# Kernel tuning notes

Hardware: AMD Instinct MI355X
Metric: run time of the kernel (lower is better)

The kernel has to match this reference:

```python
import jax, jax.numpy as jnp
import numpy as np

B, L = 4, 2048
D_MODEL, D_STATE, D_CONV, N_BLOCKS = 128, 16, 8, 6
EXPAND = 2
D_INNER = EXPAND * D_MODEL          # 256
DT_RANK = (D_MODEL + 15) // 16      # 8
CONV_K = 7                          # pre_conv kernel


def setup_inputs() -> dict:
    key = jax.random.key(0)
    ks = jax.random.split(key, 10)
    f = lambda k, s: jax.random.normal(k, s, jnp.float32)
    sc = 0.02
    A_init = jnp.broadcast_to(
        jnp.log(jnp.arange(1, D_STATE + 1, dtype=jnp.float32)),
        (N_BLOCKS, D_INNER, D_STATE)) + 0.0
    return {
        "x": f(ks[0], (B, L, 1)),
        "pre_conv_w": f(ks[1], (D_MODEL, 1, CONV_K)) * sc,
        "pre_conv_b": jnp.zeros((D_MODEL,), jnp.float32),
        "ln_w": jnp.ones((N_BLOCKS, D_MODEL), jnp.float32),
        "ln_b": jnp.zeros((N_BLOCKS, D_MODEL), jnp.float32),
        "W_in": f(ks[2], (N_BLOCKS, 2 * D_INNER, D_MODEL)) * sc,
        "conv_w": f(ks[3], (N_BLOCKS, D_INNER, 1, D_CONV)) * sc,  # depthwise OIH
        "conv_b": jnp.zeros((N_BLOCKS, D_INNER), jnp.float32),
        "W_x": f(ks[4], (N_BLOCKS, DT_RANK + 2 * D_STATE, D_INNER)) * sc,
        "W_dt": f(ks[5], (N_BLOCKS, D_INNER, DT_RANK)) * sc,
        "b_dt": jnp.full((N_BLOCKS, D_INNER), -4.6, jnp.float32),  # softplus ~ 0.01
        "A_log": A_init,
        "D_skip": jnp.ones((N_BLOCKS, D_INNER), jnp.float32),
        "W_out": f(ks[6], (N_BLOCKS, D_MODEL, D_INNER)) * sc,
        "out_w": f(ks[7], (1, D_MODEL)) * sc,
        "out_b": jnp.zeros((1,), jnp.float32),
    }


def _layernorm(x, w, b, eps=1e-5):
    m = jnp.mean(x, axis=-1, keepdims=True)
    v = jnp.mean(jnp.square(x - m), axis=-1, keepdims=True)
    return (x - m) * jax.lax.rsqrt(v + eps) * w + b


def _mamba(x, W_in, cw, cb, W_x, W_dt, b_dt, A_log, D_skip, W_out):
    # x: (B, L, D_MODEL)
    xz = jnp.einsum('bld,ed->ble', x, W_in)            # (B,L,2E)
    xi, z = jnp.split(xz, 2, axis=-1)
    # depthwise causal conv over time
    xc = jax.lax.conv_general_dilated(
        xi.transpose(0, 2, 1), cw, window_strides=(1,),
        padding=[(D_CONV - 1, 0)],
        dimension_numbers=('NCH', 'OIH', 'NCH'),
        feature_group_count=D_INNER) + cb[None, :, None]
    xc = jax.nn.silu(xc).transpose(0, 2, 1)            # (B,L,E)
    dbl = jnp.einsum('ble,re->blr', xc, W_x)
    dt = dbl[..., :DT_RANK]
    Bm = dbl[..., DT_RANK:DT_RANK + D_STATE]           # (B,L,N)
    Cm = dbl[..., DT_RANK + D_STATE:]                  # (B,L,N)
    delta = jax.nn.softplus(jnp.einsum('blr,er->ble', dt, W_dt) + b_dt)
    A = -jnp.exp(A_log)                                # (E,N)

    def step(h, inp):
        d, b, c, u = inp                               # (B,E),(B,N),(B,N),(B,E)
        h = h * jnp.exp(d[..., None] * A) + (d * u)[..., None] * b[:, None, :]
        return h, jnp.einsum('ben,bn->be', h, c)

    h0 = jnp.zeros((x.shape[0], D_INNER, D_STATE), x.dtype)
    xs = (delta.transpose(1, 0, 2), Bm.transpose(1, 0, 2),
          Cm.transpose(1, 0, 2), xc.transpose(1, 0, 2))
    _, ys = jax.lax.scan(step, h0, xs)                 # ys: (L,B,E)
    y = ys.transpose(1, 0, 2) + D_skip * xc
    y = y * jax.nn.silu(z)
    return jnp.einsum('ble,de->bld', y, W_out)


def reference(x, pre_conv_w, pre_conv_b, ln_w, ln_b, W_in, conv_w, conv_b,
              W_x, W_dt, b_dt, A_log, D_skip, W_out, out_w, out_b):
    # pre_conv (1 -> d_model), SAME padding, then exact GELU
    h = jax.lax.conv_general_dilated(
        x.transpose(0, 2, 1), pre_conv_w, window_strides=(1,),
        padding=[(CONV_K // 2, CONV_K // 2)],
        dimension_numbers=('NCH', 'OIH', 'NCH')) + pre_conv_b[None, :, None]
    h = jax.nn.gelu(h, approximate=False).transpose(0, 2, 1)  # (B,L,D)

    def block(carry, p):
        lw, lb, Wi, cw, cb, Wx, Wdt, bdt, Alog, Dsk, Wo = p
        y = _mamba(_layernorm(carry, lw, lb), Wi, cw, cb, Wx, Wdt, bdt, Alog, Dsk, Wo)
        return carry + y, None                         # dropout is identity (eval)

    h, _ = jax.lax.scan(block, h, (ln_w, ln_b, W_in, conv_w, conv_b,
                                   W_x, W_dt, b_dt, A_log, D_skip, W_out))
    return (jnp.einsum('bld,od->blo', h, out_w) + out_b)[..., 0]  # (B,L)
```

## Files before the change

kernel.cpp:

```cpp
#include <hip/hip_runtime.h>
#include <hip/hip_bf16.h>
#include <math.h>

#define BB 4
#define LL 2048
#define DM 128
#define DI 256
#define DS 16
#define DTR 8
#define NB 6
#define KPRE 7
#define KC 8
#define NC 64
#define CT 32
#define BL (BB*LL)
#define SU 4

typedef __attribute__((ext_vector_type(8))) short short8v;
typedef __attribute__((ext_vector_type(4))) float f32x4;

__global__ void k_preconv_gelu(const float* __restrict__ x,
                               const float* __restrict__ w,
                               const float* __restrict__ bias,
                               float* __restrict__ h,
                               const float* __restrict__ Wi,
                               const float* __restrict__ Wo,
                               __hip_bfloat16* __restrict__ wi,
                               __hip_bfloat16* __restrict__ wo) {
    int tid = blockIdx.x * blockDim.x + threadIdx.x;
    int d = tid & (DM - 1);
    int l = (tid >> 7) & (LL - 1);
    int b = tid >> 18;
    float acc = bias[d];
#pragma unroll
    for (int k = 0; k < KPRE; ++k) {
        int pos = l + k - 3;
        float xv = (pos >= 0 && pos < LL) ? x[b * LL + pos] : 0.f;
        acc = fmaf(xv, w[d * KPRE + k], acc);
    }
    h[tid] = 0.5f * acc * (1.f + erff(acc * 0.70710678118654752f));
    if (tid < NB * 2 * DI * DM) wi[tid] = __float2bfloat16(Wi[tid]);
    if (tid < NB * DM * DI)     wo[tid] = __float2bfloat16(Wo[tid]);
}

__global__ __launch_bounds__(256) void k_ln_gemm1(const float* __restrict__ h,
                                                  const float* __restrict__ lw,
                                                  const float* __restrict__ lb,
                                                  const __hip_bfloat16* __restrict__ W,
                                                  float* __restrict__ xz) {
    __shared__ __hip_bfloat16 As[128 * 128];
    int wave = threadIdx.x >> 6;
    int lane = threadIdx.x & 63;
    int mBase = blockIdx.x * 128;
    int nBase = blockIdx.y * 128;
    for (int it = 0; it < 32; ++it) {
        int row = wave * 32 + it;
        int t = mBase + row;
        float v0 = h[t * DM + lane];
        float v1 = h[t * DM + lane + 64];
        float s = v0 + v1;
#pragma unroll
        for (int off = 32; off; off >>= 1) s += __shfl_xor(s, off);
        float mean = s * (1.f / 128.f);
        float d0 = v0 - mean, d1 = v1 - mean;
        float q = d0 * d0 + d1 * d1;
#pragma unroll
        for (int off = 32; off; off >>= 1) q += __shfl_xor(q, off);
        float rstd = rsqrtf(q * (1.f / 128.f) + 1e-5f);
        int sw = (row & 7) << 3;
        As[row * 128 + (lane ^ sw)]        = __float2bfloat16(d0 * rstd * lw[lane] + lb[lane]);
        As[row * 128 + ((lane + 64) ^ sw)] = __float2bfloat16(d1 * rstd * lw[lane + 64] + lb[lane + 64]);
    }
    __syncthreads();
    int wm = wave & 1, wn = wave >> 1;
    int r  = lane & 15;
    int kh = lane >> 4;
    f32x4 acc[4][4] = {};
    for (int k0 = 0; k0 < DM; k0 += 32) {
        short8v af[4], bf[4];
#pragma unroll
        for (int i = 0; i < 4; ++i) {
            int row = wm * 64 + i * 16 + r;
            int cbk = (k0 >> 3) + kh;
            af[i] = *(const short8v*)&As[row * 128 + ((cbk ^ (row & 7)) << 3)];
            bf[i] = *(const short8v*)&W[(size_t)(nBase + wn * 64 + i * 16 + r) * DM + k0 + kh * 8];
        }
#pragma unroll
        for (int i = 0; i < 4; ++i)
#pragma unroll
            for (int j = 0; j < 4; ++j)
                acc[i][j] = __builtin_amdgcn_mfma_f32_16x16x32_bf16(af[i], bf[j], acc[i][j], 0, 0, 0);
    }
#pragma unroll
    for (int i = 0; i < 4; ++i)
#pragma unroll
        for (int j = 0; j < 4; ++j)
#pragma unroll
            for (int rg = 0; rg < 4; ++rg) {
                size_t off = (size_t)(mBase + wm * 64 + i * 16 + kh * 4 + rg) * (2 * DI)
                           + nBase + wn * 64 + j * 16 + r;
                xz[off] = acc[i][j][rg];
            }
}

__global__ __launch_bounds__(256) void k_gemm2_mfma(const __hip_bfloat16* __restrict__ A,
                                                    const __hip_bfloat16* __restrict__ W,
                                                    float* __restrict__ C) {
    int wave = threadIdx.x >> 6;
    int lane = threadIdx.x & 63;
    int wm = wave & 1, wn = wave >> 1;
    int mBase = blockIdx.x * 32 + wm * 16;
    int nBase = wn * 64;
    int r  = lane & 15;
    int kh = lane >> 4;
    f32x4 acc[4] = {};
    for (int k0 = 0; k0 < DI; k0 += 32) {
        short8v af = *(const short8v*)&A[(size_t)(mBase + r) * DI + k0 + kh * 8];
        short8v bf[4];
#pragma unroll
        for (int j = 0; j < 4; ++j)
            bf[j] = *(const short8v*)&W[(size_t)(nBase + j * 16 + r) * DI + k0 + kh * 8];
#pragma unroll
        for (int j = 0; j < 4; ++j)
            acc[j] = __builtin_amdgcn_mfma_f32_16x16x32_bf16(af, bf[j], acc[j], 0, 0, 0);
    }
#pragma unroll
    for (int j = 0; j < 4; ++j)
#pragma unroll
        for (int rg = 0; rg < 4; ++rg) {
            size_t off = (size_t)(mBase + kh * 4 + rg) * DM + nBase + j * 16 + r;
            C[off] += acc[j][rg];
        }
}

__global__ __launch_bounds__(256) void k_conv_wx(const float* __restrict__ xz,
                                                 const float* __restrict__ cw,
                                                 const float* __restrict__ cbs,
                                                 const float* __restrict__ Wx,
                                                 const float* __restrict__ Wdt,
                                                 const float* __restrict__ bdt,
                                                 float* __restrict__ xc,
                                                 float* __restrict__ BC,
                                                 float* __restrict__ delta) {
    int lane = threadIdx.x & 63;
    int t = blockIdx.x * 4 + (threadIdx.x >> 6);
    int tl = t & (LL - 1);
    int b = t >> 11;
    float xv[4];
#pragma unroll
    for (int j = 0; j < 4; ++j) {
        int e = lane + 64 * j;
        float4 cw0 = *(const float4*)&cw[e * KC];
        float4 cw1 = *(const float4*)&cw[e * KC + 4];
        float wts[8] = {cw0.x, cw0.y, cw0.z, cw0.w, cw1.x, cw1.y, cw1.z, cw1.w};
        float acc = cbs[e];
#pragma unroll
        for (int k = 0; k < KC; ++k) {
            int pos = tl + k - (KC - 1);
            float v = (pos >= 0) ? xz[((size_t)(b * LL + pos) << 9) + e] : 0.f;
            acc = fmaf(v, wts[k], acc);
        }
        xv[j] = acc / (1.f + __expf(-acc));
        xc[((size_t)t << 8) + e] = xv[j];
    }
    float dt[8];
    float bcv = 0.f;
#pragma unroll
    for (int o = 0; o < 40; ++o) {
        const float* w = &Wx[o * DI];
        float s = xv[0] * w[lane];
        s = fmaf(xv[1], w[lane + 64], s);
        s = fmaf(xv[2], w[lane + 128], s);
        s = fmaf(xv[3], w[lane + 192], s);
#pragma unroll
        for (int off = 32; off; off >>= 1) s += __shfl_xor(s, off);
        if (o < 8) dt[o] = s;
        else if (lane == o - 8) bcv = s;
    }
    if (lane < 32) BC[((size_t)t << 5) + lane] = bcv;
#pragma unroll
    for (int j = 0; j < 4; ++j) {
        int e = lane + 64 * j;
        float s = bdt[e];
#pragma unroll
        for (int r = 0; r < 8; ++r) s = fmaf(dt[r], Wdt[e * 8 + r], s);
        delta[((size_t)t << 8) + e] = fmaxf(s, 0.f) + log1pf(__expf(-fabsf(s)));
    }
}

__global__ __launch_bounds__(256) void k_scan1(const float* __restrict__ delta,
                                               const float* __restrict__ xc,
                                               const float* __restrict__ BC,
                                               const float* __restrict__ A_log,
                                               float* __restrict__ P,
                                               float* __restrict__ hend) {
    int blk = blockIdx.x;
    int eg = blk & 3;
    int c = (blk >> 2) & (NC - 1);
    int b = blk >> 8;
    int tid = threadIdx.x;
    int e = eg * 64 + (tid >> 2);
    int ng = tid & 3;
    float4 al = *(const float4*)&A_log[e * DS + 4 * ng];
    float Aen[4] = {-__expf(al.x), -__expf(al.y), -__expf(al.z), -__expf(al.w)};
    float h[4] = {}, Pl[4] = {1.f, 1.f, 1.f, 1.f};
    int base = b * LL + c * CT;
    const float* dp = delta + (size_t)base * DI + e;
    const float* up = xc + (size_t)base * DI + e;
    const float* bp = BC + (size_t)base * 32 + 4 * ng;
    for (int l0 = 0; l0 < CT; l0 += SU) {
        float d[SU], u[SU];
        float4 bm[SU];
#pragma unroll
        for (int j = 0; j < SU; ++j) {
            d[j]  = dp[(l0 + j) * DI];
            u[j]  = up[(l0 + j) * DI];
            bm[j] = *(const float4*)&bp[(l0 + j) * 32];
        }
#pragma unroll
        for (int j = 0; j < SU; ++j) {
            float du = d[j] * u[j];
            float a0 = __expf(d[j] * Aen[0]);
            float a1 = __expf(d[j] * Aen[1]);
            float a2 = __expf(d[j] * Aen[2]);
            float a3 = __expf(d[j] * Aen[3]);
            h[0] = fmaf(h[0], a0, du * bm[j].x);
            h[1] = fmaf(h[1], a1, du * bm[j].y);
            h[2] = fmaf(h[2], a2, du * bm[j].z);
            h[3] = fmaf(h[3], a3, du * bm[j].w);
            Pl[0] *= a0; Pl[1] *= a1; Pl[2] *= a2; Pl[3] *= a3;
        }
    }
    size_t oidx = (((size_t)(b * NC + c)) * DI + e) * DS + 4 * ng;
    *(float4*)&P[oidx]    = make_float4(Pl[0], Pl[1], Pl[2], Pl[3]);
    *(float4*)&hend[oidx] = make_float4(h[0], h[1], h[2], h[3]);
}

__global__ void k_scan_carry(const float* __restrict__ P,
                             const float* __restrict__ hend,
                             float* __restrict__ hin) {
    int tid = blockIdx.x * blockDim.x + threadIdx.x;
    int n = tid & 15;
    int e = (tid >> 4) & 255;
    int b = tid >> 12;
    float carry = 0.f;
    for (int c = 0; c < NC; ++c) {
        size_t idx = (((size_t)(b * NC + c)) * DI + e) * DS + n;
        hin[idx] = carry;
        carry = fmaf(P[idx], carry, hend[idx]);
    }
}

__global__ __launch_bounds__(256) void k_scan3(const float* __restrict__ delta,
                                               const float* __restrict__ xc,
                                               const float* __restrict__ BC,
                                               const float* __restrict__ A_log,
                                               const float* __restrict__ hin,
                                               const float* __restrict__ xz,
                                               const float* __restrict__ Dsk,
                                               __hip_bfloat16* __restrict__ y) {
    int blk = blockIdx.x;
    int eg = blk & 3;
    int c = (blk >> 2) & (NC - 1);
    int b = blk >> 8;
    int tid = threadIdx.x;
    int e = eg * 64 + (tid >> 2);
    int ng = tid & 3;
    float4 al = *(const float4*)&A_log[e * DS + 4 * ng];
    float Aen[4] = {-__expf(al.x), -__expf(al.y), -__expf(al.z), -__expf(al.w)};
    float dsk = Dsk[e];
    size_t hidx = (((size_t)(b * NC + c)) * DI + e) * DS + 4 * ng;
    float4 h4 = *(const float4*)&hin[hidx];
    float h[4] = {h4.x, h4.y, h4.z, h4.w};
    int base = b * LL + c * CT;
    const float* dp = delta + (size_t)base * DI + e;
    const float* up = xc + (size_t)base * DI + e;
    const float* bp = BC + (size_t)base * 32 + 4 * ng;
    const float* zp = xz + ((size_t)base << 9) + DI + e;
    __hip_bfloat16* yp = y + (size_t)base * DI + e;
    for (int l0 = 0; l0 < CT; l0 += SU) {
        float d[SU], u[SU], zv[SU];
        float4 bm[SU], cm[SU];
#pragma unroll
        for (int j = 0; j < SU; ++j) {
            d[j]  = dp[(l0 + j) * DI];
            u[j]  = up[(l0 + j) * DI];
            bm[j] = *(const float4*)&bp[(l0 + j) * 32];
            cm[j] = *(const float4*)&bp[(l0 + j) * 32 + 16];
            zv[j] = zp[(size_t)(l0 + j) << 9];
        }
#pragma unroll
        for (int j = 0; j < SU; ++j) {
            float du = d[j] * u[j];
            float a0 = __expf(d[j] * Aen[0]);
            float a1 = __expf(d[j] * Aen[1]);
            float a2 = __expf(d[j] * Aen[2]);
            float a3 = __expf(d[j] * Aen[3]);
            h[0] = fmaf(h[0], a0, du * bm[j].x);
            h[1] = fmaf(h[1], a1, du * bm[j].y);
            h[2] = fmaf(h[2], a2, du * bm[j].z);
            h[3] = fmaf(h[3], a3, du * bm[j].w);
            float yc = h[0] * cm[j].x;
            yc = fmaf(h[1], cm[j].y, yc);
            yc = fmaf(h[2], cm[j].z, yc);
            yc = fmaf(h[3], cm[j].w, yc);
            yc += __shfl_xor(yc, 1);
            yc += __shfl_xor(yc, 2);
            if (ng == 0) {
                float z = zv[j];
                float val = (yc + dsk * u[j]) * (z / (1.f + __expf(-z)));
                yp[(l0 + j) * DI] = __float2bfloat16(val);
            }
        }
    }
}

__global__ void k_out(const float* __restrict__ h,
                      const float* __restrict__ ow,
                      const float* __restrict__ ob,
                      float* __restrict__ out) {
    int t = blockIdx.x * 4 + (threadIdx.x >> 6);
    int lane = threadIdx.x & 63;
    float s = h[t * DM + lane] * ow[lane] + h[t * DM + lane + 64] * ow[lane + 64];
#pragma unroll
    for (int off = 32; off; off >>= 1) s += __shfl_xor(s, off);
    if (lane == 0) out[t] = s + ob[0];
}

extern "C" void kernel_launch(void* const* d_in, const int* in_sizes, int n_in,
                              void* d_out, int out_size, void* d_ws, size_t ws_size,
                              hipStream_t stream) {
    (void)in_sizes; (void)n_in; (void)out_size; (void)ws_size;
    const float* x      = (const float*)d_in[0];
    const float* pcw    = (const float*)d_in[1];
    const float* pcb    = (const float*)d_in[2];
    const float* ln_w   = (const float*)d_in[3];
    const float* ln_b   = (const float*)d_in[4];
    const float* W_in   = (const float*)d_in[5];
    const float* conv_w = (const float*)d_in[6];
    const float* conv_b = (const float*)d_in[7];
    const float* W_x    = (const float*)d_in[8];
    const float* W_dt   = (const float*)d_in[9];
    const float* b_dt   = (const float*)d_in[10];
    const float* A_log  = (const float*)d_in[11];
    const float* D_skip = (const float*)d_in[12];
    const float* W_out  = (const float*)d_in[13];
    const float* out_w  = (const float*)d_in[14];
    const float* out_b  = (const float*)d_in[15];

    float* ws    = (float*)d_ws;
    float* h     = ws;
    float* xz    = h     + (size_t)BL * DM;
    float* xc    = xz    + (size_t)BL * 2 * DI;
    float* BC    = xc    + (size_t)BL * DI;
    float* delta = BC    + (size_t)BL * 2 * DS;
    float* P     = delta + (size_t)BL * DI;
    float* hend  = P     + (size_t)BB * NC * DI * DS;
    float* hin   = hend  + (size_t)BB * NC * DI * DS;
    __hip_bfloat16* y_bf  = (__hip_bfloat16*)(hin + (size_t)BB * NC * DI * DS);
    __hip_bfloat16* wi_bf = y_bf  + (size_t)BL * DI;
    __hip_bfloat16* wo_bf = wi_bf + (size_t)NB * 2 * DI * DM;

    k_preconv_gelu<<<(BB * LL * DM) / 256, 256, 0, stream>>>(
        x, pcw, pcb, h, W_in, W_out, wi_bf, wo_bf);

    for (int blk = 0; blk < NB; ++blk) {
        k_ln_gemm1<<<dim3(BL / 128, (2 * DI) / 128), 256, 0, stream>>>(
            h, ln_w + blk * DM, ln_b + blk * DM, wi_bf + (size_t)blk * 2 * DI * DM, xz);
        k_conv_wx<<<BL / 4, 256, 0, stream>>>(
            xz, conv_w + (size_t)blk * DI * KC, conv_b + blk * DI,
            W_x + (size_t)blk * 40 * DI, W_dt + (size_t)blk * DI * DTR,
            b_dt + blk * DI, xc, BC, delta);
        k_scan1<<<BB * NC * 4, 256, 0, stream>>>(
            delta, xc, BC, A_log + (size_t)blk * DI * DS, P, hend);
        k_scan_carry<<<(BB * DI * DS) / 256, 256, 0, stream>>>(P, hend, hin);
        k_scan3<<<BB * NC * 4, 256, 0, stream>>>(
            delta, xc, BC, A_log + (size_t)blk * DI * DS, hin, xz,
            D_skip + blk * DI, y_bf);
        k_gemm2_mfma<<<BL / 32, 256, 0, stream>>>(
            y_bf, wo_bf + (size_t)blk * DM * DI, h);
    }

    k_out<<<BL / 4, 256, 0, stream>>>(h, out_w, out_b, (float*)d_out);
}
```

Before: 618.7 us.

## Fuse all stages into one cooperative persistent kernel with grid syncs

Replaces the 38 separate kernel launches with a single cooperative persistent kernel that loops over work items for each stage and separates stages with grid-wide barriers. GEMM tiles are reshaped to 512 work units each (64x128 for in-projection, 16x128 for out-projection) to match a grid capped at 512 blocks. The aim is to remove launch overhead and inter-kernel gaps. In exchange it adds grid-sync costs and limits occupancy to co-resident blocks, and a fallback path of separate kernels is kept for when cooperative launch is unavailable.

```diff
diff --git a/kernel.cpp b/kernel.cpp
--- a/kernel.cpp
+++ b/kernel.cpp
@@ -1,6 +1,9 @@
 #include <hip/hip_runtime.h>
 #include <hip/hip_bf16.h>
+#include <hip/hip_cooperative_groups.h>
 #include <math.h>
+
+namespace cg = cooperative_groups;
 
 #define BB 4
 #define LL 2048
@@ -19,18 +22,14 @@
 typedef __attribute__((ext_vector_type(8))) short short8v;
 typedef __attribute__((ext_vector_type(4))) float f32x4;
 
-__global__ void k_preconv_gelu(const float* __restrict__ x,
-                               const float* __restrict__ w,
-                               const float* __restrict__ bias,
-                               float* __restrict__ h,
-                               const float* __restrict__ Wi,
-                               const float* __restrict__ Wo,
-                               __hip_bfloat16* __restrict__ wi,
-                               __hip_bfloat16* __restrict__ wo) {
-    int tid = blockIdx.x * blockDim.x + threadIdx.x;
-    int d = tid & (DM - 1);
-    int l = (tid >> 7) & (LL - 1);
-    int b = tid >> 18;
+
+__device__ __forceinline__ void dev_preconv(int idx,
+    const float* __restrict__ x, const float* __restrict__ w, const float* __restrict__ bias,
+    float* __restrict__ h, const float* __restrict__ Wi, const float* __restrict__ Wo,
+    __hip_bfloat16* __restrict__ wi, __hip_bfloat16* __restrict__ wo) {
+    int d = idx & (DM - 1);
+    int l = (idx >> 7) & (LL - 1);
+    int b = idx >> 18;
     float acc = bias[d];
 #pragma unroll
     for (int k = 0; k < KPRE; ++k) {
@@ -38,23 +37,19 @@
         float xv = (pos >= 0 && pos < LL) ? x[b * LL + pos] : 0.f;
         acc = fmaf(xv, w[d * KPRE + k], acc);
     }
-    h[tid] = 0.5f * acc * (1.f + erff(acc * 0.70710678118654752f));
-    if (tid < NB * 2 * DI * DM) wi[tid] = __float2bfloat16(Wi[tid]);
-    if (tid < NB * DM * DI)     wo[tid] = __float2bfloat16(Wo[tid]);
-}
-
-__global__ __launch_bounds__(256) void k_ln_gemm1(const float* __restrict__ h,
-                                                  const float* __restrict__ lw,
-                                                  const float* __restrict__ lb,
-                                                  const __hip_bfloat16* __restrict__ W,
-                                                  float* __restrict__ xz) {
-    __shared__ __hip_bfloat16 As[128 * 128];
-    int wave = threadIdx.x >> 6;
-    int lane = threadIdx.x & 63;
-    int mBase = blockIdx.x * 128;
-    int nBase = blockIdx.y * 128;
-    for (int it = 0; it < 32; ++it) {
-        int row = wave * 32 + it;
+    h[idx] = 0.5f * acc * (1.f + erff(acc * 0.70710678118654752f));
+    if (idx < NB * 2 * DI * DM) wi[idx] = __float2bfloat16(Wi[idx]);
+    if (idx < NB * DM * DI)     wo[idx] = __float2bfloat16(Wo[idx]);
+}
+
+__device__ __forceinline__ void dev_ln_gemm1(int v, int wave, int lane,
+    const float* __restrict__ h, const float* __restrict__ lw, const float* __restrict__ lb,
+    const __hip_bfloat16* __restrict__ W, float* __restrict__ xz,
+    __hip_bfloat16* As) {
+    int tileM = v >> 2, tileN = v & 3;
+    int mBase = tileM * 64, nBase = tileN * 128;
+    for (int it = 0; it < 16; ++it) {
+        int row = wave * 16 + it;
         int t = mBase + row;
         float v0 = h[t * DM + lane];
         float v1 = h[t * DM + lane + 64];
@@ -72,78 +67,43 @@
         As[row * 128 + ((lane + 64) ^ sw)] = __float2bfloat16(d1 * rstd * lw[lane + 64] + lb[lane + 64]);
     }
     __syncthreads();
-    int wm = wave & 1, wn = wave >> 1;
     int r  = lane & 15;
     int kh = lane >> 4;
-    f32x4 acc[4][4] = {};
+    f32x4 acc[4][2] = {};
     for (int k0 = 0; k0 < DM; k0 += 32) {
-        short8v af[4], bf[4];
+        short8v af[4], bf[2];
 #pragma unroll
         for (int i = 0; i < 4; ++i) {
-            int row = wm * 64 + i * 16 + r;
+            int row = i * 16 + r;
             int cbk = (k0 >> 3) + kh;
             af[i] = *(const short8v*)&As[row * 128 + ((cbk ^ (row & 7)) << 3)];
-            bf[i] = *(const short8v*)&W[(size_t)(nBase + wn * 64 + i * 16 + r) * DM + k0 + kh * 8];
-        }
+        }
+#pragma unroll
+        for (int j = 0; j < 2; ++j)
+            bf[j] = *(const short8v*)&W[(size_t)(nBase + wave * 32 + j * 16 + r) * DM + k0 + kh * 8];
 #pragma unroll
         for (int i = 0; i < 4; ++i)
 #pragma unroll
-            for (int j = 0; j < 4; ++j)
+            for (int j = 0; j < 2; ++j)
                 acc[i][j] = __builtin_amdgcn_mfma_f32_16x16x32_bf16(af[i], bf[j], acc[i][j], 0, 0, 0);
     }
 #pragma unroll
     for (int i = 0; i < 4; ++i)
 #pragma unroll
-        for (int j = 0; j < 4; ++j)
+        for (int j = 0; j < 2; ++j)
 #pragma unroll
             for (int rg = 0; rg < 4; ++rg) {
-                size_t off = (size_t)(mBase + wm * 64 + i * 16 + kh * 4 + rg) * (2 * DI)
-                           + nBase + wn * 64 + j * 16 + r;
+                size_t off = (size_t)(mBase + i * 16 + kh * 4 + rg) * (2 * DI)
+                           + nBase + wave * 32 + j * 16 + r;
                 xz[off] = acc[i][j][rg];
             }
-}
-
-__global__ __launch_bounds__(256) void k_gemm2_mfma(const __hip_bfloat16* __restrict__ A,
-                                                    const __hip_bfloat16* __restrict__ W,
-                                                    float* __restrict__ C) {
-    int wave = threadIdx.x >> 6;
-    int lane = threadIdx.x & 63;
-    int wm = wave & 1, wn = wave >> 1;
-    int mBase = blockIdx.x * 32 + wm * 16;
-    int nBase = wn * 64;
-    int r  = lane & 15;
-    int kh = lane >> 4;
-    f32x4 acc[4] = {};
-    for (int k0 = 0; k0 < DI; k0 += 32) {
-        short8v af = *(const short8v*)&A[(size_t)(mBase + r) * DI + k0 + kh * 8];
-        short8v bf[4];
-#pragma unroll
-        for (int j = 0; j < 4; ++j)
-            bf[j] = *(const short8v*)&W[(size_t)(nBase + j * 16 + r) * DI + k0 + kh * 8];
-#pragma unroll
-        for (int j = 0; j < 4; ++j)
-            acc[j] = __builtin_amdgcn_mfma_f32_16x16x32_bf16(af, bf[j], acc[j], 0, 0, 0);
-    }
-#pragma unroll
-    for (int j = 0; j < 4; ++j)
-#pragma unroll
-        for (int rg = 0; rg < 4; ++rg) {
-            size_t off = (size_t)(mBase + kh * 4 + rg) * DM + nBase + j * 16 + r;
-            C[off] += acc[j][rg];
-        }
-}
-
-__global__ __launch_bounds__(256) void k_conv_wx(const float* __restrict__ xz,
-                                                 const float* __restrict__ cw,
-                                                 const float* __restrict__ cbs,
-                                                 const float* __restrict__ Wx,
-                                                 const float* __restrict__ Wdt,
-                                                 const float* __restrict__ bdt,
-                                                 float* __restrict__ xc,
-                                                 float* __restrict__ BC,
-                                                 float* __restrict__ delta) {
-    int lane = threadIdx.x & 63;
-    int t = blockIdx.x * 4 + (threadIdx.x >> 6);
+    __syncthreads();
+}
+
+__device__ __forceinline__ void dev_conv_wx(int t, int lane,
+    const float* __restrict__ xz, const float* __restrict__ cw, const float* __restrict__ cbs,
+    const float* __restrict__ Wx, const float* __restrict__ Wdt, const float* __restrict__ bdt,
+    float* __restrict__ xc, float* __restrict__ BC, float* __restrict__ delta) {
     int tl = t & (LL - 1);
     int b = t >> 11;
     float xv[4];
@@ -188,17 +148,12 @@
     }
 }
 
-__global__ __launch_bounds__(256) void k_scan1(const float* __restrict__ delta,
-                                               const float* __restrict__ xc,
-                                               const float* __restrict__ BC,
-                                               const float* __restrict__ A_log,
-                                               float* __restrict__ P,
-                                               float* __restrict__ hend) {
-    int blk = blockIdx.x;
+__device__ __forceinline__ void dev_scan1(int blk, int tid,
+    const float* __restrict__ delta, const float* __restrict__ xc, const float* __restrict__ BC,
+    const float* __restrict__ A_log, float* __restrict__ P, float* __restrict__ hend) {
     int eg = blk & 3;
     int c = (blk >> 2) & (NC - 1);
     int b = blk >> 8;
-    int tid = threadIdx.x;
     int e = eg * 64 + (tid >> 2);
     int ng = tid & 3;
     float4 al = *(const float4*)&A_log[e * DS + 4 * ng];
@@ -236,13 +191,11 @@
     *(float4*)&hend[oidx] = make_float4(h[0], h[1], h[2], h[3]);
 }
 
-__global__ void k_scan_carry(const float* __restrict__ P,
-                             const float* __restrict__ hend,
-                             float* __restrict__ hin) {
-    int tid = blockIdx.x * blockDim.x + threadIdx.x;
-    int n = tid & 15;
-    int e = (tid >> 4) & 255;
-    int b = tid >> 12;
+__device__ __forceinline__ void dev_carry(int gtid,
+    const float* __restrict__ P, const float* __restrict__ hend, float* __restrict__ hin) {
+    int n = gtid & 15;
+    int e = (gtid >> 4) & 255;
+    int b = gtid >> 12;
     float carry = 0.f;
     for (int c = 0; c < NC; ++c) {
         size_t idx = (((size_t)(b * NC + c)) * DI + e) * DS + n;
@@ -251,19 +204,13 @@
     }
 }
 
-__global__ __launch_bounds__(256) void k_scan3(const float* __restrict__ delta,
-                                               const float* __restrict__ xc,
-                                               const float* __restrict__ BC,
-                                               const float* __restrict__ A_log,
-                                               const float* __restrict__ hin,
-                                               const float* __restrict__ xz,
-                                               const float* __restrict__ Dsk,
-                                               __hip_bfloat16* __restrict__ y) {
-    int blk = blockIdx.x;
+__device__ __forceinline__ void dev_scan3(int blk, int tid,
+    const float* __restrict__ delta, const float* __restrict__ xc, const float* __restrict__ BC,
+    const float* __restrict__ A_log, const float* __restrict__ hin, const float* __restrict__ xz,
+    const float* __restrict__ Dsk, __hip_bfloat16* __restrict__ y) {
     int eg = blk & 3;
     int c = (blk >> 2) & (NC - 1);
     int b = blk >> 8;
-    int tid = threadIdx.x;
     int e = eg * 64 + (tid >> 2);
     int ng = tid & 3;
     float4 al = *(const float4*)&A_log[e * DS + 4 * ng];
@@ -315,16 +262,125 @@
     }
 }
 
-__global__ void k_out(const float* __restrict__ h,
-                      const float* __restrict__ ow,
-                      const float* __restrict__ ob,
-                      float* __restrict__ out) {
-    int t = blockIdx.x * 4 + (threadIdx.x >> 6);
-    int lane = threadIdx.x & 63;
+__device__ __forceinline__ void dev_gemm2(int v, int wave, int lane,
+    const __hip_bfloat16* __restrict__ A, const __hip_bfloat16* __restrict__ W,
+    float* __restrict__ C) {
+    int mBase = v * 16;
+    int r  = lane & 15;
+    int kh = lane >> 4;
+    f32x4 acc[2] = {};
+    for (int k0 = 0; k0 < DI; k0 += 32) {
+        short8v af = *(const short8v*)&A[(size_t)(mBase + r) * DI + k0 + kh * 8];
+        short8v bf[2];
+#pragma unroll
+        for (int j = 0; j < 2; ++j)
+            bf[j] = *(const short8v*)&W[(size_t)(wave * 32 + j * 16 + r) * DI + k0 + kh * 8];
+#pragma unroll
+        for (int j = 0; j < 2; ++j)
+            acc[j] = __builtin_amdgcn_mfma_f32_16x16x32_bf16(af, bf[j], acc[j], 0, 0, 0);
+    }
+#pragma unroll
+    for (int j = 0; j < 2; ++j)
+#pragma unroll
+        for (int rg = 0; rg < 4; ++rg) {
+            size_t off = (size_t)(mBase + kh * 4 + rg) * DM + wave * 32 + j * 16 + r;
+            C[off] += acc[j][rg];
+        }
+}
+
+__device__ __forceinline__ void dev_out(int t, int lane,
+    const float* __restrict__ h, const float* __restrict__ ow, const float* __restrict__ ob,
+    float* __restrict__ out) {
     float s = h[t * DM + lane] * ow[lane] + h[t * DM + lane + 64] * ow[lane + 64];
 #pragma unroll
     for (int off = 32; off; off >>= 1) s += __shfl_xor(s, off);
     if (lane == 0) out[t] = s + ob[0];
+}
+
+
+struct MegaArgs {
+    const float *x, *pcw, *pcb, *ln_w, *ln_b, *W_in, *conv_w, *conv_b;
+    const float *W_x, *W_dt, *b_dt, *A_log, *D_skip, *W_out, *out_w, *out_b;
+    float *h, *xz, *xc, *BC, *delta, *P, *hend, *hin, *out;
+    __hip_bfloat16 *y_bf, *wi_bf, *wo_bf;
+};
+
+__global__ __launch_bounds__(256) void k_mega(MegaArgs a) {
+    __shared__ __hip_bfloat16 As[64 * 128];
+    cg::grid_group g = cg::this_grid();
+    int bid = blockIdx.x, tid = threadIdx.x;
+    int nb = gridDim.x;
+    int wave = tid >> 6, lane = tid & 63;
+
+    for (int v = bid; v < (BB * LL * DM) / 256; v += nb)
+        dev_preconv(v * 256 + tid, a.x, a.pcw, a.pcb, a.h, a.W_in, a.W_out, a.wi_bf, a.wo_bf);
+    g.sync();
+
+    for (int blk = 0; blk < NB; ++blk) {
+        for (int v = bid; v < 512; v += nb)
+            dev_ln_gemm1(v, wave, lane, a.h, a.ln_w + blk * DM, a.ln_b + blk * DM,
+                         a.wi_bf + (size_t)blk * 2 * DI * DM, a.xz, As);
+        g.sync();
+        for (int v = bid; v < BL / 4; v += nb)
+            dev_conv_wx(v * 4 + wave, lane, a.xz, a.conv_w + (size_t)blk * DI * KC,
+                        a.conv_b + blk * DI, a.W_x + (size_t)blk * 40 * DI,
+                        a.W_dt + (size_t)blk * DI * DTR, a.b_dt + blk * DI,
+                        a.xc, a.BC, a.delta);
+        g.sync();
+        for (int v = bid; v < BB * NC * 4; v += nb)
+            dev_scan1(v, tid, a.delta, a.xc, a.BC, a.A_log + (size_t)blk * DI * DS, a.P, a.hend);
+        g.sync();
+        for (int v = bid; v < (BB * DI * DS) / 256; v += nb)
+            dev_carry(v * 256 + tid, a.P, a.hend, a.hin);
+        g.sync();
+        for (int v = bid; v < BB * NC * 4; v += nb)
+            dev_scan3(v, tid, a.delta, a.xc, a.BC, a.A_log + (size_t)blk * DI * DS,
+                      a.hin, a.xz, a.D_skip + blk * DI, a.y_bf);
+        g.sync();
+        for (int v = bid; v < 512; v += nb)
+            dev_gemm2(v, wave, lane, a.y_bf, a.wo_bf + (size_t)blk * DM * DI, a.h);
+        g.sync();
+    }
+
+    for (int v = bid; v < BL / 4; v += nb)
+        dev_out(v * 4 + wave, lane, a.h, a.out_w, a.out_b, a.out);
+}
+
+
+__global__ void w_preconv(const float* x, const float* w, const float* bias, float* h,
+                          const float* Wi, const float* Wo,
+                          __hip_bfloat16* wi, __hip_bfloat16* wo) {
+    dev_preconv(blockIdx.x * 256 + threadIdx.x, x, w, bias, h, Wi, Wo, wi, wo);
+}
+__global__ __launch_bounds__(256) void w_ln_gemm1(const float* h, const float* lw, const float* lb,
+                                                  const __hip_bfloat16* W, float* xz) {
+    __shared__ __hip_bfloat16 As[64 * 128];
+    dev_ln_gemm1(blockIdx.x, threadIdx.x >> 6, threadIdx.x & 63, h, lw, lb, W, xz, As);
+}
+__global__ __launch_bounds__(256) void w_conv_wx(const float* xz, const float* cw, const float* cbs,
+                                                 const float* Wx, const float* Wdt, const float* bdt,
+                                                 float* xc, float* BC, float* delta) {
+    dev_conv_wx(blockIdx.x * 4 + (threadIdx.x >> 6), threadIdx.x & 63,
+                xz, cw, cbs, Wx, Wdt, bdt, xc, BC, delta);
+}
+__global__ __launch_bounds__(256) void w_scan1(const float* delta, const float* xc, const float* BC,
+                                               const float* A_log, float* P, float* hend) {
+    dev_scan1(blockIdx.x, threadIdx.x, delta, xc, BC, A_log, P, hend);
+}
+__global__ void w_carry(const float* P, const float* hend, float* hin) {
+    dev_carry(blockIdx.x * 256 + threadIdx.x, P, hend, hin);
+}
+__global__ __launch_bounds__(256) void w_scan3(const float* delta, const float* xc, const float* BC,
+                                               const float* A_log, const float* hin, const float* xz,
+                                               const float* Dsk, __hip_bfloat16* y) {
+    dev_scan3(blockIdx.x, threadIdx.x, delta, xc, BC, A_log, hin, xz, Dsk, y);
+}
+__global__ __launch_bounds__(256) void w_gemm2(const __hip_bfloat16* A, const __hip_bfloat16* W,
+                                               float* C) {
+    dev_gemm2(blockIdx.x, threadIdx.x >> 6, threadIdx.x & 63, A, W, C);
+}
+__global__ void w_out(const float* h, const float* ow, const float* ob, float* out) {
+    dev_out(blockIdx.x * 4 + (threadIdx.x >> 6), threadIdx.x & 63, h, ow, ob, out);
 }
 
 extern "C" void kernel_launch(void* const* d_in, const int* in_sizes, int n_in,
@@ -361,25 +417,45 @@
     __hip_bfloat16* wi_bf = y_bf  + (size_t)BL * DI;
     __hip_bfloat16* wo_bf = wi_bf + (size_t)NB * 2 * DI * DM;
 
-    k_preconv_gelu<<<(BB * LL * DM) / 256, 256, 0, stream>>>(
-        x, pcw, pcb, h, W_in, W_out, wi_bf, wo_bf);
-
-    for (int blk = 0; blk < NB; ++blk) {
-        k_ln_gemm1<<<dim3(BL / 128, (2 * DI) / 128), 256, 0, stream>>>(
-            h, ln_w + blk * DM, ln_b + blk * DM, wi_bf + (size_t)blk * 2 * DI * DM, xz);
-        k_conv_wx<<<BL / 4, 256, 0, stream>>>(
-            xz, conv_w + (size_t)blk * DI * KC, conv_b + blk * DI,
-            W_x + (size_t)blk * 40 * DI, W_dt + (size_t)blk * DI * DTR,
-            b_dt + blk * DI, xc, BC, delta);
-        k_scan1<<<BB * NC * 4, 256, 0, stream>>>(
-            delta, xc, BC, A_log + (size_t)blk * DI * DS, P, hend);
-        k_scan_carry<<<(BB * DI * DS) / 256, 256, 0, stream>>>(P, hend, hin);
-        k_scan3<<<BB * NC * 4, 256, 0, stream>>>(
-            delta, xc, BC, A_log + (size_t)blk * DI * DS, hin, xz,
-            D_skip + blk * DI, y_bf);
-        k_gemm2_mfma<<<BL / 32, 256, 0, stream>>>(
-            y_bf, wo_bf + (size_t)blk * DM * DI, h);
-    }
-
-    k_out<<<BL / 4, 256, 0, stream>>>(h, out_w, out_b, (float*)d_out);
-}
+    int dev = 0;
+    (void)hipGetDevice(&dev);
+    int coopAttr = 0;
+    (void)hipDeviceGetAttribute(&coopAttr, hipDeviceAttributeCooperativeLaunch, dev);
+    int numCU = 0;
+    (void)hipDeviceGetAttribute(&numCU, hipDeviceAttributeMultiprocessorCount, dev);
+    int maxBpCU = 0;
+    (void)hipOccupancyMaxActiveBlocksPerMultiprocessor(&maxBpCU, k_mega, 256, 0);
+    int grid = maxBpCU * numCU;
+    if (grid > 512) grid = 512;
+
+    bool launched = false;
+    if (coopAttr && grid > 0) {
+        MegaArgs ma = {x, pcw, pcb, ln_w, ln_b, W_in, conv_w, conv_b,
+                       W_x, W_dt, b_dt, A_log, D_skip, W_out, out_w, out_b,
+                       h, xz, xc, BC, delta, P, hend, hin, (float*)d_out,
+                       y_bf, wi_bf, wo_bf};
+        void* kp[] = {&ma};
+        hipError_t e = hipLaunchCooperativeKernel((void*)k_mega, dim3(grid), dim3(256), kp, 0, stream);
+        launched = (e == hipSuccess);
+        if (!launched) (void)hipGetLastError();
+    }
+
+    if (!launched) {
+        w_preconv<<<(BB * LL * DM) / 256, 256, 0, stream>>>(x, pcw, pcb, h, W_in, W_out, wi_bf, wo_bf);
+        for (int blk = 0; blk < NB; ++blk) {
+            w_ln_gemm1<<<512, 256, 0, stream>>>(
+                h, ln_w + blk * DM, ln_b + blk * DM, wi_bf + (size_t)blk * 2 * DI * DM, xz);
+            w_conv_wx<<<BL / 4, 256, 0, stream>>>(
+                xz, conv_w + (size_t)blk * DI * KC, conv_b + blk * DI,
+                W_x + (size_t)blk * 40 * DI, W_dt + (size_t)blk * DI * DTR,
+                b_dt + blk * DI, xc, BC, delta);
+            w_scan1<<<BB * NC * 4, 256, 0, stream>>>(
+                delta, xc, BC, A_log + (size_t)blk * DI * DS, P, hend);
+            w_carry<<<(BB * DI * DS) / 256, 256, 0, stream>>>(P, hend, hin);
+            w_scan3<<<BB * NC * 4, 256, 0, stream>>>(
+                delta, xc, BC, A_log + (size_t)blk * DI * DS, hin, xz, D_skip + blk * DI, y_bf);
+            w_gemm2<<<BL / 16, 256, 0, stream>>>(y_bf, wo_bf + (size_t)blk * DM * DI, h);
+        }
+        w_out<<<BL / 4, 256, 0, stream>>>(h, out_w, out_b, (float*)d_out);
+    }
+}
```

New measurement: 565.3 us. 1.09x faster.
